# Optimization experiments

Hardware: AMD Instinct MI355X
Metric: run time of the kernel (lower is better)

The kernel has to match this reference:

```python
import jax, jax.numpy as jnp
import numpy as np

B, S, D, H, L, V, C = 8, 1024, 768, 12, 6, 32000, 2
HD = D // H
DF = 3072
MAX_POS = 2048
EPS = 1e-5


def layer_norm(x, scale, bias):
    m = jnp.mean(x, axis=-1, keepdims=True)
    v = jnp.mean((x - m) ** 2, axis=-1, keepdims=True)
    return (x - m) / jnp.sqrt(v + EPS) * scale + bias


def setup_inputs() -> dict:
    key = jax.random.key(0)
    ks = jax.random.split(key, 16)
    std = 0.02
    return {
        "input_ids": jax.random.randint(ks[0], (B, S), 0, V),
        "attention_mask": jax.random.randint(ks[1], (B, S), 0, 2),
        "token_emb": jax.random.normal(ks[2], (V, D), jnp.float32) * std,
        "pos_emb": jax.random.normal(ks[3], (MAX_POS, D), jnp.float32) * std,
        "qkv_w": jax.random.normal(ks[4], (L, D, 3 * D), jnp.float32) * std,
        "qkv_b": jnp.zeros((L, 3 * D), jnp.float32),
        "out_w": jax.random.normal(ks[5], (L, D, D), jnp.float32) * std,
        "out_b": jnp.zeros((L, D), jnp.float32),
        "n1_s": jnp.ones((L, D), jnp.float32),
        "n1_b": jnp.zeros((L, D), jnp.float32),
        "ff1_w": jax.random.normal(ks[6], (L, D, DF), jnp.float32) * std,
        "ff1_b": jnp.zeros((L, DF), jnp.float32),
        "ff2_w": jax.random.normal(ks[7], (L, DF, D), jnp.float32) * std,
        "ff2_b": jnp.zeros((L, D), jnp.float32),
        "n2_s": jnp.ones((L, D), jnp.float32),
        "n2_b": jnp.zeros((L, D), jnp.float32),
        "hln_s": jnp.ones((D,), jnp.float32),
        "hln_b": jnp.zeros((D,), jnp.float32),
        "cls_w": jax.random.normal(ks[8], (D, C), jnp.float32) * std,
        "cls_b": jnp.zeros((C,), jnp.float32),
    }


def reference(input_ids, attention_mask, token_emb, pos_emb, qkv_w, qkv_b,
              out_w, out_b, n1_s, n1_b, ff1_w, ff1_b, ff2_w, ff2_b,
              n2_s, n2_b, hln_s, hln_b, cls_w, cls_b):
    # embeddings: token + position, scaled by sqrt(d_model)
    x = (token_emb[input_ids] + pos_emb[:S][None, :, :]) * np.float32(np.sqrt(D))
    # extended mask: 0 at valid tokens, -10000 at padding -> (B,1,1,S)
    ext = (1.0 - attention_mask.astype(x.dtype))[:, None, None, :] * -10000.0
    scale = np.float32(1.0 / np.sqrt(HD))
    for i in range(L):
        # --- self attention (pre-norm) ---
        h = layer_norm(x, n1_s[i], n1_b[i])
        qkv = (h @ qkv_w[i] + qkv_b[i]).reshape(B, S, H, 3, HD)
        q, k, v = qkv[..., 0, :], qkv[..., 1, :], qkv[..., 2, :]  # (B,S,H,HD)
        scores = jnp.einsum('bshd,bthd->bhst', q, k) * scale
        # faithful to source: masked_fill(ext_mask == 0, -1e9)
        scores = jnp.where(ext == 0, jnp.asarray(-1e9, scores.dtype), scores)
        w = jax.nn.softmax(scores, axis=-1)
        att = jnp.einsum('bhst,bthd->bshd', w, v).reshape(B, S, D)
        x = x + (att @ out_w[i] + out_b[i])
        # --- feed forward (pre-norm) ---
        h2 = layer_norm(x, n2_s[i], n2_b[i])
        ff = jax.nn.relu(h2 @ ff1_w[i] + ff1_b[i]) @ ff2_w[i] + ff2_b[i]
        x = x + ff
    # CLS pooling head
    pooled = layer_norm(x[:, 0, :], hln_s, hln_b)
    return pooled @ cls_w + cls_b
```

## Files before the change

kernel.cpp:

```cpp
#include <hip/hip_runtime.h>
#include <hip/hip_bf16.h>

typedef unsigned short u16;
typedef __bf16 bf16x8 __attribute__((ext_vector_type(8)));
typedef float f32x4 __attribute__((ext_vector_type(4)));
typedef unsigned int u32x4 __attribute__((ext_vector_type(4)));

#define DEVI __device__ __forceinline__

typedef __attribute__((address_space(3))) void lds_void;
typedef __attribute__((address_space(1))) const void gbl_void;

DEVI void gload16(const void* gp, void* lp) {
    __builtin_amdgcn_global_load_lds((gbl_void*)gp, (lds_void*)lp, 16, 0, 0);
}

DEVI u16 f2b(float f) {
    unsigned int u = __builtin_bit_cast(unsigned int, f);
    unsigned int lsb = (u >> 16) & 1u;
    u += 0x7fffu + lsb;
    return (u16)(u >> 16);
}
DEVI float b2f(u16 b) {
    unsigned int u = ((unsigned int)b) << 16;
    return __builtin_bit_cast(float, u);
}

DEVI float fexp2(float x) {
#if __has_builtin(__builtin_amdgcn_exp2f)
    return __builtin_amdgcn_exp2f(x);
#else
    return __expf(x * 0.6931471805599453f);
#endif
}

DEVI void swz_block(int& bx, int& by, int& bz) {
    const int gx = gridDim.x, gy = gridDim.y;
    const int nwg2 = gx * gy;
    int hw = blockIdx.x + gx * blockIdx.y;
    int id = (nwg2 & 7) ? hw : ((hw & 7) * (nwg2 >> 3) + (hw >> 3));
    bx = id % gx;
    by = id / gx;
    bz = blockIdx.z;
}

DEVI float blockReduceSum(float v, float* red, int tid) {
    #pragma unroll
    for (int o = 32; o; o >>= 1) v += __shfl_xor(v, o);
    __syncthreads();
    if ((tid & 63) == 0) red[tid >> 6] = v;
    __syncthreads();
    return red[0] + red[1] + red[2] + red[3];
}

__global__ void detect_kernel(const void* tok, int* flag) {
    __shared__ int bad;
    if (threadIdx.x == 0) bad = 0;
    __syncthreads();
    const u16* p = (const u16*)tok;
    int cnt = 0;
    for (int j = 0; j < 16; ++j) {
        float v = b2f(p[2 * (threadIdx.x * 16 + j)]);
        if (!(fabsf(v) < 1.0f)) cnt++;
    }
    if (cnt) atomicAdd(&bad, 1);
    __syncthreads();
    if (threadIdx.x == 0) flag[0] = (bad == 0) ? 1 : 0;
}

__global__ void to_f32_kernel(const void* src, float* dst, int n, const int* flag) {
    int i = blockIdx.x * 256 + threadIdx.x;
    if (i >= n) return;
    if (flag[0]) dst[i] = b2f(((const u16*)src)[i]);
    else         dst[i] = ((const float*)src)[i];
}

DEVI void gemm_core_async(const u16* __restrict__ A, int lda,
                          const u16* __restrict__ Bt, int ldb,
                          int K, f32x4 (&acc)[4][4],
                          u16* As, u16* Bs)
{
    const int tid  = threadIdx.x;
    const int lane = tid & 63;
    const int wave = tid >> 6;
    const int quad = lane >> 4;
    const int l16  = lane & 15;
    const int wm   = wave >> 1;
    const int wn   = wave & 1;

    const int c0 = (wave * 2 + 0) * 64 + lane;
    const int c1 = (wave * 2 + 1) * 64 + lane;
    const int r0 = c0 >> 2, h0 = (c0 & 3) * 8;
    const int r1 = c1 >> 2, h1 = (c1 & 3) * 8;

    for (int k0 = 0; k0 < K; k0 += 32) {
        __syncthreads();
        gload16(A  + (size_t)r0 * lda + k0 + h0, As + c0 * 8);
        gload16(Bt + (size_t)r0 * ldb + k0 + h0, Bs + c0 * 8);
        gload16(A  + (size_t)r1 * lda + k0 + h1, As + c1 * 8);
        gload16(Bt + (size_t)r1 * ldb + k0 + h1, Bs + c1 * 8);
        __syncthreads();

        bf16x8 af[4], bfv[4];
        #pragma unroll
        for (int mt = 0; mt < 4; ++mt)
            af[mt] = *(const bf16x8*)(As + (wm * 64 + mt * 16 + l16) * 32 + quad * 8);
        #pragma unroll
        for (int nt = 0; nt < 4; ++nt)
            bfv[nt] = *(const bf16x8*)(Bs + (wn * 64 + nt * 16 + l16) * 32 + quad * 8);
        #pragma unroll
        for (int mt = 0; mt < 4; ++mt)
            #pragma unroll
            for (int nt = 0; nt < 4; ++nt)
                acc[mt][nt] = __builtin_amdgcn_mfma_f32_16x16x32_bf16(af[mt], bfv[nt], acc[mt][nt], 0, 0, 0);
    }
}

template<int EPI>
__global__ __launch_bounds__(256) void gemm_std(
    const u16* __restrict__ A, int lda,
    const u16* __restrict__ Bt, int ldb,
    const float* __restrict__ bias,
    u16* __restrict__ outB, int ldc, int K)
{
    __shared__ u16 As[128 * 32];
    __shared__ u16 Bs[128 * 32];
    int bx, by, bz;
    swz_block(bx, by, bz);
    const size_t bM = (size_t)by * 128;
    const size_t bN = (size_t)bx * 128;
    f32x4 acc[4][4] = {};
    gemm_core_async(A + bM * lda, lda, Bt + bN * ldb, ldb, K, acc, As, Bs);

    const int tid = threadIdx.x, lane = tid & 63, wave = tid >> 6;
    const int wm = wave >> 1, wn = wave & 1, quad = lane >> 4, l16 = lane & 15;
    #pragma unroll
    for (int mt = 0; mt < 4; ++mt)
        #pragma unroll
        for (int nt = 0; nt < 4; ++nt) {
            size_t col = bN + wn * 64 + nt * 16 + l16;
            float bcol = bias[col];
            #pragma unroll
            for (int r = 0; r < 4; ++r) {
                size_t row = bM + wm * 64 + mt * 16 + quad * 4 + r;
                float v = acc[mt][nt][r] + bcol;
                if constexpr (EPI == 1) v = fmaxf(v, 0.f);
                outB[row * ldc + col] = f2b(v);
            }
        }
}

__global__ __launch_bounds__(256) void gemm_splitk(
    const u16* __restrict__ A, int lda,
    const u16* __restrict__ Bt, int ldb,
    const float* __restrict__ bias,
    float* __restrict__ resid, int ldc, int Ksub)
{
    __shared__ u16 As[128 * 32];
    __shared__ u16 Bs[128 * 32];
    int bx, by, bz;
    swz_block(bx, by, bz);
    const size_t bM = (size_t)by * 128;
    const size_t bN = (size_t)bx * 128;
    const int Koff = bz * Ksub;
    f32x4 acc[4][4] = {};
    gemm_core_async(A + bM * lda + Koff, lda, Bt + bN * ldb + Koff, ldb, Ksub, acc, As, Bs);

    const int tid = threadIdx.x, lane = tid & 63, wave = tid >> 6;
    const int wm = wave >> 1, wn = wave & 1, quad = lane >> 4, l16 = lane & 15;
    const bool addb = (bz == 0);
    #pragma unroll
    for (int mt = 0; mt < 4; ++mt)
        #pragma unroll
        for (int nt = 0; nt < 4; ++nt) {
            size_t col = bN + wn * 64 + nt * 16 + l16;
            float bcol = addb ? bias[col] : 0.f;
            #pragma unroll
            for (int r = 0; r < 4; ++r) {
                size_t row = bM + wm * 64 + mt * 16 + quad * 4 + r;
                atomicAdd(&resid[row * ldc + col], acc[mt][nt][r] + bcol);
            }
        }
}

__global__ __launch_bounds__(256, 2) void flash_attn(
    const u16* __restrict__ qkv, const u16* __restrict__ vt,
    const int* __restrict__ mask, u16* __restrict__ attout)
{
    __shared__ u16 Ks[128 * 64];
    __shared__ u16 Vs[64 * 128];
    __shared__ u16 Ps[128 * 64];
    __shared__ u16 Msb[1024];

    const int bh = blockIdx.y;
    const int b = bh / 12, h = bh % 12;
    const int q0 = blockIdx.x * 128;
    const int tid = threadIdx.x, lane = tid & 63, wave = tid >> 6;
    const int quad = lane >> 4, l16 = lane & 15;
    const int sw = l16 & 7;

    for (int i = tid; i < 1024; i += 256)
        Msb[i] = (mask[b * 1024 + i] != 0) ? f2b(-1e9f) : (u16)0;

    bf16x8 aq[2][2];
    #pragma unroll
    for (int mt = 0; mt < 2; ++mt)
        #pragma unroll
        for (int s = 0; s < 2; ++s)
            aq[mt][s] = *(const bf16x8*)(qkv + (size_t)(b * 1024 + q0 + wave * 32 + mt * 16 + l16) * 2304
                                          + h * 192 + s * 32 + quad * 8);

    const float SC2 = 0.18033688011112042f;

    float mi[2][4], li[2][4];
    f32x4 Oacc[2][4] = {};
    #pragma unroll
    for (int mt = 0; mt < 2; ++mt)
        #pragma unroll
        for (int r = 0; r < 4; ++r) { mi[mt][r] = -3e38f; li[mt][r] = 0.f; }

    for (int kt = 0; kt < 8; ++kt) {
        u32x4 kreg[4], vreg[4];
        #pragma unroll
        for (int i = 0; i < 4; ++i) {
            int id = i * 256 + tid, row = id >> 3, ch = id & 7;
            kreg[i] = *(const u32x4*)(qkv + (size_t)(b * 1024 + kt * 128 + row) * 2304 + h * 192 + 64 + ch * 8);
        }
        #pragma unroll
        for (int i = 0; i < 4; ++i) {
            int id = i * 256 + tid, row = id >> 4, ch = id & 15;
            vreg[i] = *(const u32x4*)(vt + (size_t)bh * 65536 + (size_t)row * 1024 + kt * 128 + ch * 8);
        }
        __syncthreads();
        #pragma unroll
        for (int i = 0; i < 4; ++i) {
            int id = i * 256 + tid, row = id >> 3, ch = id & 7;
            *(u32x4*)(Ks + row * 64 + ((ch ^ (row & 7)) * 8)) = kreg[i];
        }
        #pragma unroll
        for (int i = 0; i < 4; ++i) {
            int id = i * 256 + tid, row = id >> 4, ch = id & 15;
            *(u32x4*)(Vs + row * 128 + ((ch ^ (row & 7)) * 8)) = vreg[i];
        }
        __syncthreads();

        f32x4 Sacc[2][8] = {};
        #pragma unroll
        for (int s = 0; s < 2; ++s) {
            bf16x8 kf[8];
            #pragma unroll
            for (int nt = 0; nt < 8; ++nt)
                kf[nt] = *(const bf16x8*)(Ks + (nt * 16 + l16) * 64 + (((s * 4 + quad) ^ sw) * 8));
            #pragma unroll
            for (int mt = 0; mt < 2; ++mt)
                #pragma unroll
                for (int nt = 0; nt < 8; ++nt)
                    Sacc[mt][nt] = __builtin_amdgcn_mfma_f32_16x16x32_bf16(aq[mt][s], kf[nt], Sacc[mt][nt], 0, 0, 0);
        }

        float bias[8];
        #pragma unroll
        for (int nt = 0; nt < 8; ++nt) bias[nt] = b2f(Msb[kt * 128 + nt * 16 + l16]);
        #pragma unroll
        for (int mt = 0; mt < 2; ++mt)
            #pragma unroll
            for (int nt = 0; nt < 8; ++nt)
                #pragma unroll
                for (int r = 0; r < 4; ++r)
                    Sacc[mt][nt][r] = fmaf(Sacc[mt][nt][r], SC2, bias[nt]);

        #pragma unroll
        for (int mt = 0; mt < 2; ++mt) {
            float al[4];
            #pragma unroll
            for (int r = 0; r < 4; ++r) {
                float rm = fmaxf(
                    fmaxf(fmaxf(Sacc[mt][0][r], Sacc[mt][1][r]), fmaxf(Sacc[mt][2][r], Sacc[mt][3][r])),
                    fmaxf(fmaxf(Sacc[mt][4][r], Sacc[mt][5][r]), fmaxf(Sacc[mt][6][r], Sacc[mt][7][r])));
                #pragma unroll
                for (int o = 8; o; o >>= 1) rm = fmaxf(rm, __shfl_xor(rm, o));
                float mn = fmaxf(mi[mt][r], rm);
                al[r] = fexp2(mi[mt][r] - mn);
                mi[mt][r] = mn;
                float rs = 0.f;
                #pragma unroll
                for (int nt = 0; nt < 8; ++nt) {
                    float pv = fexp2(Sacc[mt][nt][r] - mn);
                    rs += pv;
                    Sacc[mt][nt][r] = pv;
                }
                #pragma unroll
                for (int o = 8; o; o >>= 1) rs += __shfl_xor(rs, o);
                li[mt][r] = li[mt][r] * al[r] + rs;
            }
            #pragma unroll
            for (int ntv = 0; ntv < 4; ++ntv)
                #pragma unroll
                for (int r = 0; r < 4; ++r) Oacc[mt][ntv][r] *= al[r];
        }

        #pragma unroll
        for (int hf = 0; hf < 2; ++hf) {
            #pragma unroll
            for (int mt = 0; mt < 2; ++mt) {
                const int rowb = wave * 32 + mt * 16 + quad * 4;
                #pragma unroll
                for (int n4 = 0; n4 < 4; ++n4) {
                    const int slot = n4 * 2 + (l16 >> 3);
                    #pragma unroll
                    for (int r = 0; r < 4; ++r) {
                        const int row = rowb + r;
                        Ps[row * 64 + ((slot ^ (row & 7)) * 8) + sw] = f2b(Sacc[mt][hf * 4 + n4][r]);
                    }
                }
            }
            #pragma unroll
            for (int s2h = 0; s2h < 2; ++s2h) {
                const int s2 = hf * 2 + s2h;
                bf16x8 vf[4];
                #pragma unroll
                for (int ntv = 0; ntv < 4; ++ntv)
                    vf[ntv] = *(const bf16x8*)(Vs + (ntv * 16 + l16) * 128 + (((s2 * 4 + quad) ^ sw) * 8));
                #pragma unroll
                for (int mt2 = 0; mt2 < 2; ++mt2) {
                    bf16x8 pf = *(const bf16x8*)(Ps + (wave * 32 + mt2 * 16 + l16) * 64 + (((s2h * 4 + quad) ^ sw) * 8));
                    #pragma unroll
                    for (int ntv = 0; ntv < 4; ++ntv)
                        Oacc[mt2][ntv] = __builtin_amdgcn_mfma_f32_16x16x32_bf16(pf, vf[ntv], Oacc[mt2][ntv], 0, 0, 0);
                }
            }
        }
    }

    #pragma unroll
    for (int mt = 0; mt < 2; ++mt)
        #pragma unroll
        for (int r = 0; r < 4; ++r) {
            float inv = 1.0f / li[mt][r];
            int s = q0 + wave * 32 + mt * 16 + quad * 4 + r;
            #pragma unroll
            for (int ntv = 0; ntv < 4; ++ntv)
                attout[((size_t)(b * 1024 + s)) * 768 + h * 64 + ntv * 16 + l16] = f2b(Oacc[mt][ntv][r] * inv);
        }
}

__global__ __launch_bounds__(256) void embed_kernel(
    const int* __restrict__ ids, const void* __restrict__ tok,
    const void* __restrict__ pos, float* __restrict__ x, const int* __restrict__ flag)
{
    const int e  = blockIdx.x * 256 + threadIdx.x;
    const int bs = e / 192;
    const int d  = (e - bs * 192) * 4;
    const int s  = bs & 1023;
    const int id = ids[bs];
    float t[4], p4[4];
    if (flag[0]) {
        const u16* tb = (const u16*)tok + (size_t)id * 768 + d;
        const u16* pb = (const u16*)pos + (size_t)s  * 768 + d;
        #pragma unroll
        for (int j = 0; j < 4; ++j) { t[j] = b2f(tb[j]); p4[j] = b2f(pb[j]); }
    } else {
        const float* tb = (const float*)tok + (size_t)id * 768 + d;
        const float* pb = (const float*)pos + (size_t)s  * 768 + d;
        #pragma unroll
        for (int j = 0; j < 4; ++j) { t[j] = tb[j]; p4[j] = pb[j]; }
    }
    float* xo = x + (size_t)bs * 768 + d;
    #pragma unroll
    for (int j = 0; j < 4; ++j) xo[j] = (t[j] + p4[j]) * 27.7128129211020f;
}

__global__ __launch_bounds__(256) void layernorm_kernel(
    const float* __restrict__ x, const float* __restrict__ sc,
    const float* __restrict__ bi, u16* __restrict__ out)
{
    __shared__ float red[4];
    const size_t row = blockIdx.x;
    const float* xr = x + row * 768;
    const int tid = threadIdx.x;
    float v0 = xr[tid], v1 = xr[tid + 256], v2 = xr[tid + 512];
    float s = blockReduceSum(v0 + v1 + v2, red, tid);
    float mean = s * (1.0f / 768.0f);
    float d0 = v0 - mean, d1 = v1 - mean, d2 = v2 - mean;
    float q = blockReduceSum(d0 * d0 + d1 * d1 + d2 * d2, red, tid);
    float rstd = rsqrtf(q * (1.0f / 768.0f) + 1e-5f);
    u16* orow = out + row * 768;
    orow[tid]       = f2b(d0 * rstd * sc[tid]       + bi[tid]);
    orow[tid + 256] = f2b(d1 * rstd * sc[tid + 256] + bi[tid + 256]);
    orow[tid + 512] = f2b(d2 * rstd * sc[tid + 512] + bi[tid + 512]);
}

__global__ __launch_bounds__(256) void transpose_w_kernel(
    const void* __restrict__ W, size_t off, u16* __restrict__ Wt,
    int Kd, int Nd, const int* __restrict__ flag)
{
    __shared__ u16 tile[32][34];
    const int n0 = blockIdx.x * 32, k0 = blockIdx.y * 32;
    const int tx = threadIdx.x & 31, ty = threadIdx.x >> 5;
    const int fl = flag[0];
    #pragma unroll
    for (int i = 0; i < 4; ++i) {
        size_t idx = off + (size_t)(k0 + ty + i * 8) * Nd + n0 + tx;
        u16 val = fl ? ((const u16*)W)[idx] : f2b(((const float*)W)[idx]);
        tile[ty + i * 8][tx] = val;
    }
    __syncthreads();
    #pragma unroll
    for (int i = 0; i < 4; ++i)
        Wt[(size_t)(n0 + ty + i * 8) * Kd + k0 + tx] = tile[tx][ty + i * 8];
}

__global__ __launch_bounds__(256) void build_vt_kernel(
    const u16* __restrict__ qkv, u16* __restrict__ vt)
{
    __shared__ u16 tile[64][72];
    const int bh = blockIdx.y;
    const int b = bh / 12, h = bh % 12;
    const int t0 = blockIdx.x * 64;
    const int tid = threadIdx.x;
    const int tl = tid >> 2;
    const int d4 = (tid & 3) * 16;
    const u16* src = qkv + (size_t)(b * 1024 + t0 + tl) * 2304 + h * 192 + 128 + d4;
    *(u32x4*)(&tile[tl][d4])     = *(const u32x4*)(src);
    *(u32x4*)(&tile[tl][d4 + 8]) = *(const u32x4*)(src + 8);
    __syncthreads();
    const int dd = tid >> 2;
    const int tstart = (tid & 3) * 16;
    union { u16 us[16]; u32x4 v[2]; } pk;
    #pragma unroll
    for (int j = 0; j < 16; ++j) pk.us[j] = tile[tstart + j][dd];
    u16* dst = vt + ((size_t)bh * 64 + dd) * 1024 + t0 + tstart;
    *(u32x4*)(dst)     = pk.v[0];
    *(u32x4*)(dst + 8) = pk.v[1];
}

__global__ __launch_bounds__(256) void pooled_cls_kernel(
    const float* __restrict__ x, const float* __restrict__ hs, const float* __restrict__ hb,
    const float* __restrict__ cw, const float* __restrict__ cb, void* __restrict__ dout,
    const int* __restrict__ flag)
{
    __shared__ float red[4];
    __shared__ float pooled[768];
    const int b = blockIdx.x;
    const float* xr = x + (size_t)b * 1024 * 768;
    const int tid = threadIdx.x;
    float v0 = xr[tid], v1 = xr[tid + 256], v2 = xr[tid + 512];
    float s = blockReduceSum(v0 + v1 + v2, red, tid);
    float mean = s * (1.0f / 768.0f);
    float d0 = v0 - mean, d1 = v1 - mean, d2 = v2 - mean;
    float q = blockReduceSum(d0 * d0 + d1 * d1 + d2 * d2, red, tid);
    float rstd = rsqrtf(q * (1.0f / 768.0f) + 1e-5f);
    pooled[tid]       = d0 * rstd * hs[tid]       + hb[tid];
    pooled[tid + 256] = d1 * rstd * hs[tid + 256] + hb[tid + 256];
    pooled[tid + 512] = d2 * rstd * hs[tid + 512] + hb[tid + 512];
    __syncthreads();
    float p0 = 0.f, p1 = 0.f;
    for (int c = tid; c < 768; c += 256) {
        float pv = pooled[c];
        p0 += pv * cw[2 * c];
        p1 += pv * cw[2 * c + 1];
    }
    p0 = blockReduceSum(p0, red, tid);
    p1 = blockReduceSum(p1, red, tid);
    if (tid == 0) {
        float o0 = p0 + cb[0], o1 = p1 + cb[1];
        if (flag[0]) {
            ((u16*)dout)[b * 2 + 0] = f2b(o0);
            ((u16*)dout)[b * 2 + 1] = f2b(o1);
        } else {
            ((float*)dout)[b * 2 + 0] = o0;
            ((float*)dout)[b * 2 + 1] = o1;
        }
    }
}

extern "C" void kernel_launch(void* const* d_in, const int* in_sizes, int n_in,
                              void* d_out, int out_size, void* d_ws, size_t ws_size,
                              hipStream_t stream)
{
    const int* ids  = (const int*)d_in[0];
    const int* mask = (const int*)d_in[1];
    const void* tok   = d_in[2];
    const void* pos   = d_in[3];
    const void* qkv_w = d_in[4];
    const void* qkv_b = d_in[5];
    const void* out_w = d_in[6];
    const void* out_b = d_in[7];
    const void* n1_s  = d_in[8];
    const void* n1_b  = d_in[9];
    const void* ff1_w = d_in[10];
    const void* ff1_b = d_in[11];
    const void* ff2_w = d_in[12];
    const void* ff2_b = d_in[13];
    const void* n2_s  = d_in[14];
    const void* n2_b  = d_in[15];
    const void* hln_s = d_in[16];
    const void* hln_b = d_in[17];
    const void* cls_w = d_in[18];
    const void* cls_b = d_in[19];

    char* p = (char*)d_ws;
    auto alloc = [&](size_t bytes) -> char* {
        char* r = p; p += (bytes + 255) & ~(size_t)255; return r;
    };
    float* x      = (float*)alloc(6291456ull * 4);
    u16*   h      = (u16*)  alloc(6291456ull * 2);
    u16*   qkvB   = (u16*)  alloc(18874368ull * 2);
    u16*   vt     = (u16*)  alloc(6291456ull * 2);
    u16*   ffmid  = (u16*)  alloc(25165824ull * 2);
    u16*   wqkvT  = (u16*)  alloc(1769472ull * 2);
    u16*   woutT  = (u16*)  alloc(589824ull * 2);
    u16*   wff1T  = (u16*)  alloc(2359296ull * 2);
    u16*   wff2T  = (u16*)  alloc(2359296ull * 2);
    float* params = (float*)alloc(62978ull * 4);
    int*   flag   = (int*)  alloc(256);
    u16*   attout = h;

    float* P_qkv_b = params + 0;
    float* P_out_b = params + 13824;
    float* P_n1_s  = params + 18432;
    float* P_n1_b  = params + 23040;
    float* P_ff1_b = params + 27648;
    float* P_ff2_b = params + 46080;
    float* P_n2_s  = params + 50688;
    float* P_n2_b  = params + 55296;
    float* P_hln_s = params + 59904;
    float* P_hln_b = params + 60672;
    float* P_cls_w = params + 61440;
    float* P_cls_b = params + 62976;

    detect_kernel<<<1, 256, 0, stream>>>(tok, flag);

    auto cvt = [&](const void* src, float* dst, int n) {
        to_f32_kernel<<<(n + 255) / 256, 256, 0, stream>>>(src, dst, n, flag);
    };
    cvt(qkv_b, P_qkv_b, 13824);  cvt(out_b, P_out_b, 4608);
    cvt(n1_s,  P_n1_s,  4608);   cvt(n1_b,  P_n1_b,  4608);
    cvt(ff1_b, P_ff1_b, 18432);  cvt(ff2_b, P_ff2_b, 4608);
    cvt(n2_s,  P_n2_s,  4608);   cvt(n2_b,  P_n2_b,  4608);
    cvt(hln_s, P_hln_s, 768);    cvt(hln_b, P_hln_b, 768);
    cvt(cls_w, P_cls_w, 1536);   cvt(cls_b, P_cls_b, 2);

    embed_kernel<<<6144, 256, 0, stream>>>(ids, tok, pos, x, flag);

    for (int l = 0; l < 6; ++l) {
        transpose_w_kernel<<<dim3(72, 24), 256, 0, stream>>>(qkv_w, (size_t)l * 1769472, wqkvT, 768, 2304, flag);
        transpose_w_kernel<<<dim3(24, 24), 256, 0, stream>>>(out_w, (size_t)l * 589824,  woutT, 768, 768,  flag);
        transpose_w_kernel<<<dim3(96, 24), 256, 0, stream>>>(ff1_w, (size_t)l * 2359296, wff1T, 768, 3072, flag);
        transpose_w_kernel<<<dim3(24, 96), 256, 0, stream>>>(ff2_w, (size_t)l * 2359296, wff2T, 3072, 768, flag);

        layernorm_kernel<<<8192, 256, 0, stream>>>(x, P_n1_s + l * 768, P_n1_b + l * 768, h);
        gemm_std<0><<<dim3(18, 64), 256, 0, stream>>>(h, 768, wqkvT, 768,
                                                      P_qkv_b + l * 2304, qkvB, 2304, 768);
        build_vt_kernel<<<dim3(16, 96), 256, 0, stream>>>(qkvB, vt);
        flash_attn<<<dim3(8, 96), 256, 0, stream>>>(qkvB, vt, mask, attout);
        gemm_splitk<<<dim3(6, 64, 2), 256, 0, stream>>>(attout, 768, woutT, 768,
                                                        P_out_b + l * 768, x, 768, 384);
        layernorm_kernel<<<8192, 256, 0, stream>>>(x, P_n2_s + l * 768, P_n2_b + l * 768, h);
        gemm_std<1><<<dim3(24, 64), 256, 0, stream>>>(h, 768, wff1T, 768,
                                                      P_ff1_b + l * 3072, ffmid, 3072, 768);
        gemm_splitk<<<dim3(6, 64, 2), 256, 0, stream>>>(ffmid, 3072, wff2T, 3072,
                                                        P_ff2_b + l * 768, x, 768, 1536);
    }
    pooled_cls_kernel<<<8, 256, 0, stream>>>(x, P_hln_s, P_hln_b, P_cls_w, P_cls_b, d_out, flag);
}
```

Measured before the change: 2.383 ms.

## Replace split-K atomic residual adds with partial buffers reduced inside layernorm

The split-K GEMMs for the output projection and FF2 now write their two K-halves to separate fp32 partial buffers, which reuse the ffmid and qkvB scratch space, instead of atomically adding into the residual stream. The next layernorm, or the pooled classifier at the end, sums the residual with both partials, writes the updated residual back and then normalizes. This removes global float atomics. In exchange, each partial is written in full and read back, which adds fp32 memory traffic. The code also depends on the scratch buffers not being overwritten before the partials are consumed.

Measured after the change: 2.174 ms. 1.1x faster.

```diff
diff --git a/kernel.cpp b/kernel.cpp
--- a/kernel.cpp
+++ b/kernel.cpp
@@ -150,11 +150,11 @@
         }
 }
 
-__global__ __launch_bounds__(256) void gemm_splitk(
+__global__ __launch_bounds__(256) void gemm_partial(
     const u16* __restrict__ A, int lda,
     const u16* __restrict__ Bt, int ldb,
     const float* __restrict__ bias,
-    float* __restrict__ resid, int ldc, int Ksub)
+    float* __restrict__ part, size_t pstride, int ldc, int Ksub)
 {
     __shared__ u16 As[128 * 32];
     __shared__ u16 Bs[128 * 32];
@@ -166,6 +166,7 @@
     f32x4 acc[4][4] = {};
     gemm_core_async(A + bM * lda + Koff, lda, Bt + bN * ldb + Koff, ldb, Ksub, acc, As, Bs);
 
+    float* __restrict__ P = part + (size_t)bz * pstride;
     const int tid = threadIdx.x, lane = tid & 63, wave = tid >> 6;
     const int wm = wave >> 1, wn = wave & 1, quad = lane >> 4, l16 = lane & 15;
     const bool addb = (bz == 0);
@@ -178,7 +179,7 @@
             #pragma unroll
             for (int r = 0; r < 4; ++r) {
                 size_t row = bM + wm * 64 + mt * 16 + quad * 4 + r;
-                atomicAdd(&resid[row * ldc + col], acc[mt][nt][r] + bcol);
+                P[row * ldc + col] = acc[mt][nt][r] + bcol;
             }
         }
 }
@@ -371,14 +372,23 @@
 }
 
 __global__ __launch_bounds__(256) void layernorm_kernel(
-    const float* __restrict__ x, const float* __restrict__ sc,
-    const float* __restrict__ bi, u16* __restrict__ out)
+    float* __restrict__ x, const float* __restrict__ part,
+    const float* __restrict__ sc, const float* __restrict__ bi,
+    u16* __restrict__ out)
 {
     __shared__ float red[4];
     const size_t row = blockIdx.x;
-    const float* xr = x + row * 768;
+    float* xr = x + row * 768;
     const int tid = threadIdx.x;
     float v0 = xr[tid], v1 = xr[tid + 256], v2 = xr[tid + 512];
+    if (part) {
+        const float* p0 = part + row * 768;
+        const float* p1 = p0 + 6291456;
+        v0 += p0[tid]       + p1[tid];
+        v1 += p0[tid + 256] + p1[tid + 256];
+        v2 += p0[tid + 512] + p1[tid + 512];
+        xr[tid] = v0; xr[tid + 256] = v1; xr[tid + 512] = v2;
+    }
     float s = blockReduceSum(v0 + v1 + v2, red, tid);
     float mean = s * (1.0f / 768.0f);
     float d0 = v0 - mean, d1 = v1 - mean, d2 = v2 - mean;
@@ -435,7 +445,8 @@
 }
 
 __global__ __launch_bounds__(256) void pooled_cls_kernel(
-    const float* __restrict__ x, const float* __restrict__ hs, const float* __restrict__ hb,
+    const float* __restrict__ x, const float* __restrict__ part,
+    const float* __restrict__ hs, const float* __restrict__ hb,
     const float* __restrict__ cw, const float* __restrict__ cb, void* __restrict__ dout,
     const int* __restrict__ flag)
 {
@@ -443,8 +454,12 @@
     __shared__ float pooled[768];
     const int b = blockIdx.x;
     const float* xr = x + (size_t)b * 1024 * 768;
+    const float* p0 = part + (size_t)b * 1024 * 768;
+    const float* p1 = p0 + 6291456;
     const int tid = threadIdx.x;
-    float v0 = xr[tid], v1 = xr[tid + 256], v2 = xr[tid + 512];
+    float v0 = xr[tid]       + p0[tid]       + p1[tid];
+    float v1 = xr[tid + 256] + p0[tid + 256] + p1[tid + 256];
+    float v2 = xr[tid + 512] + p0[tid + 512] + p1[tid + 512];
     float s = blockReduceSum(v0 + v1 + v2, red, tid);
     float mean = s * (1.0f / 768.0f);
     float d0 = v0 - mean, d1 = v1 - mean, d2 = v2 - mean;
@@ -454,16 +469,16 @@
     pooled[tid + 256] = d1 * rstd * hs[tid + 256] + hb[tid + 256];
     pooled[tid + 512] = d2 * rstd * hs[tid + 512] + hb[tid + 512];
     __syncthreads();
-    float p0 = 0.f, p1 = 0.f;
+    float q0 = 0.f, q1 = 0.f;
     for (int c = tid; c < 768; c += 256) {
         float pv = pooled[c];
-        p0 += pv * cw[2 * c];
-        p1 += pv * cw[2 * c + 1];
-    }
-    p0 = blockReduceSum(p0, red, tid);
-    p1 = blockReduceSum(p1, red, tid);
+        q0 += pv * cw[2 * c];
+        q1 += pv * cw[2 * c + 1];
+    }
+    q0 = blockReduceSum(q0, red, tid);
+    q1 = blockReduceSum(q1, red, tid);
     if (tid == 0) {
-        float o0 = p0 + cb[0], o1 = p1 + cb[1];
+        float o0 = q0 + cb[0], o1 = q1 + cb[1];
         if (flag[0]) {
             ((u16*)dout)[b * 2 + 0] = f2b(o0);
             ((u16*)dout)[b * 2 + 1] = f2b(o1);
@@ -516,6 +531,9 @@
     int*   flag   = (int*)  alloc(256);
     u16*   attout = h;
 
+    float* Apart = (float*)ffmid;
+    float* Fpart = (float*)qkvB;
+
     float* P_qkv_b = params + 0;
     float* P_out_b = params + 13824;
     float* P_n1_s  = params + 18432;
@@ -549,18 +567,20 @@
         transpose_w_kernel<<<dim3(96, 24), 256, 0, stream>>>(ff1_w, (size_t)l * 2359296, wff1T, 768, 3072, flag);
         transpose_w_kernel<<<dim3(24, 96), 256, 0, stream>>>(ff2_w, (size_t)l * 2359296, wff2T, 3072, 768, flag);
 
-        layernorm_kernel<<<8192, 256, 0, stream>>>(x, P_n1_s + l * 768, P_n1_b + l * 768, h);
+        layernorm_kernel<<<8192, 256, 0, stream>>>(x, (l == 0) ? nullptr : Fpart,
+                                                   P_n1_s + l * 768, P_n1_b + l * 768, h);
         gemm_std<0><<<dim3(18, 64), 256, 0, stream>>>(h, 768, wqkvT, 768,
                                                       P_qkv_b + l * 2304, qkvB, 2304, 768);
         build_vt_kernel<<<dim3(16, 96), 256, 0, stream>>>(qkvB, vt);
         flash_attn<<<dim3(8, 96), 256, 0, stream>>>(qkvB, vt, mask, attout);
-        gemm_splitk<<<dim3(6, 64, 2), 256, 0, stream>>>(attout, 768, woutT, 768,
-                                                        P_out_b + l * 768, x, 768, 384);
-        layernorm_kernel<<<8192, 256, 0, stream>>>(x, P_n2_s + l * 768, P_n2_b + l * 768, h);
+        gemm_partial<<<dim3(6, 64, 2), 256, 0, stream>>>(attout, 768, woutT, 768,
+                                                         P_out_b + l * 768, Apart, 6291456, 768, 384);
+        layernorm_kernel<<<8192, 256, 0, stream>>>(x, Apart,
+                                                   P_n2_s + l * 768, P_n2_b + l * 768, h);
         gemm_std<1><<<dim3(24, 64), 256, 0, stream>>>(h, 768, wff1T, 768,
                                                       P_ff1_b + l * 3072, ffmid, 3072, 768);
-        gemm_splitk<<<dim3(6, 64, 2), 256, 0, stream>>>(ffmid, 3072, wff2T, 3072,
-                                                        P_ff2_b + l * 768, x, 768, 1536);
-    }
-    pooled_cls_kernel<<<8, 256, 0, stream>>>(x, P_hln_s, P_hln_b, P_cls_w, P_cls_b, d_out, flag);
-}
+        gemm_partial<<<dim3(6, 64, 2), 256, 0, stream>>>(ffmid, 3072, wff2T, 3072,
+                                                         P_ff2_b + l * 768, Fpart, 6291456, 768, 1536);
+    }
+    pooled_cls_kernel<<<8, 256, 0, stream>>>(x, Fpart, P_hln_s, P_hln_b, P_cls_w, P_cls_b, d_out, flag);
+}
```
